# Kernel tuning notes

Hardware: AMD Instinct MI355X
Metric: run time of the kernel (lower is better)

Reference implementation:

```python
import jax, jax.numpy as jnp
import numpy as np

B, N, C, K1, K2, TD = 4, 4096, 128, 16, 8, 64
CIN = 2 * (3 + C)  # 262


def setup_inputs() -> dict:
    key = jax.random.key(0)
    ks = jax.random.split(key, 8)
    s = 0.05
    feature = jax.random.normal(ks[0], (B, C, N), jnp.float32)
    xyz = jax.random.normal(ks[1], (B, 3, N), jnp.float32)
    wq = jax.random.normal(ks[2], (TD, CIN), jnp.float32) * s
    wk = jax.random.normal(ks[3], (TD, CIN), jnp.float32) * s
    wv = jax.random.normal(ks[4], (TD, CIN), jnp.float32) * s
    w1 = jax.random.normal(ks[5], (C, TD), jnp.float32) * s
    bq = jnp.zeros((TD,), jnp.float32)
    bk = jnp.zeros((TD,), jnp.float32)
    bv = jnp.zeros((TD,), jnp.float32)
    b1 = jnp.zeros((C,), jnp.float32)
    return {"feature": feature, "xyz": xyz, "wq": wq, "bq": bq,
            "wk": wk, "bk": bk, "wv": wv, "bv": bv, "w1": w1, "b1": b1}


def _group(x, ind):
    # x: [B, Cx, N], ind: [B, N, K] -> [B, Cx, K, N]; g[b,c,k,n] = x[b,c,ind[b,n,k]]
    g = jnp.take_along_axis(x[:, :, None, :], ind[:, None, :, :], axis=3)  # [B,Cx,N,K]
    return g.transpose(0, 1, 3, 2)


def reference(feature, xyz, wq, bq, wk, bk, wv, bv, w1, b1):
    # --- KNN (self-included then dropped), idx[b,n,k] = k-th nearest of point n ---
    sq = jnp.sum(xyz * xyz, axis=1)                                   # [B,N]
    dist = sq[:, :, None] + sq[:, None, :] - 2.0 * jnp.einsum('bdn,bdm->bnm', xyz, xyz)
    _, idx = jax.lax.top_k(-dist, K1 + 1)                             # [B,N,17]
    idx = idx[:, :, 1:]                                               # drop self -> [B,N,16]
    idx1 = idx[:, :, :K2]                                             # [B,N,8]

    gxyz = _group(xyz, idx)        # [B,3,16,N]
    gxyz1 = _group(xyz, idx1)      # [B,3,8,N]
    gfea = _group(feature, idx)    # [B,C,16,N]
    gfea1 = _group(feature, idx1)  # [B,C,8,N]

    rel_xyz = gxyz - xyz[:, :, None, :]
    rel_xyz1 = gxyz1 - xyz[:, :, None, :]
    rel_fea = gfea - feature[:, :, None, :]
    rel_fea1 = gfea1 - feature[:, :, None, :]

    def relpos(rx, rf, K):
        return jnp.concatenate([
            rx,
            jnp.broadcast_to(xyz[:, :, None, :], (B, 3, K, N)),
            rf,
            jnp.broadcast_to(feature[:, :, None, :], (B, C, K, N)),
        ], axis=1)  # [B,262,K,N]

    rel_pos = relpos(rel_xyz, rel_fea, K1)     # [B,262,16,N]
    rel_pos1 = relpos(rel_xyz1, rel_fea1, K2)  # [B,262,8,N]

    # 1x1 Conv2d projections
    q = jnp.einsum('oc,bckn->bokn', wq, rel_pos1) + bq[None, :, None, None]  # [B,64,8,N]
    k = jnp.einsum('oc,bckn->bokn', wk, rel_pos) + bk[None, :, None, None]   # [B,64,16,N]
    v = jnp.einsum('oc,bckn->bokn', wv, rel_pos) + bv[None, :, None, None]   # [B,64,16,N]

    attn = jnp.einsum('bmnf,bmjf->bnjf', q, k)   # [B,8,16,N]
    attn = jax.nn.softmax(attn, axis=-2)         # softmax over j (16 neighbors)
    res = jnp.einsum('bnjf,bmjf->bmf', attn, v)  # [B,64,N]

    out = jnp.einsum('om,bmf->bof', w1, res) + b1[None, :, None]  # Conv1d 64->128
    return out + feature
```

## Files before the change

kernel.cpp:

```cpp
#include <hip/hip_runtime.h>

#define NN 4096
#define CCH 128

__global__ __launch_bounds__(256) void transpose_w(
    const float* __restrict__ wq, const float* __restrict__ wk, const float* __restrict__ wv,
    const float* __restrict__ w1,
    float* __restrict__ wTq, float* __restrict__ wTk, float* __restrict__ wTv,
    float* __restrict__ w1T, float* __restrict__ wPack) {
  int t = blockIdx.x * 256 + threadIdx.x;
  if (t < 64 * 262) {
    int o = t / 262, c = t - o * 262;
    wTq[c * 64 + o] = wq[t];
    wTk[c * 64 + o] = wk[t];
    wTv[c * 64 + o] = wv[t];
  }
  if (t < 128 * 64) {
    int r = t >> 6, c2 = t & 63;
    w1T[c2 * 128 + r] = w1[t];
  }
  if (t < 49152) {
    int r = t & 3, o = (t >> 2) & 63;
    int g = t >> 8;
    int ct = g / 6, mh = g - ct * 6;
    int m = mh >> 1, h = mh & 1;
    const float* wsrc = (m == 0) ? wq : ((m == 1) ? wk : wv);
    wPack[t] = wsrc[o * 262 + (h ? 134 : 6) + 4 * ct + r];
  }
}

__global__ __launch_bounds__(1024, 4) void knn_kernel(const float* __restrict__ xyz,
                                                      int* __restrict__ idxout) {
  __shared__ float4 pts[NN];
  __shared__ float sdist[16 * 16 * 64];
  __shared__ unsigned long long hits[32 * 64];
  __shared__ int cnt[64];
  const int b  = blockIdx.x >> 6;
  const int n0 = (blockIdx.x & 63) << 6;
  const float* xb = xyz + (size_t)b * 3 * NN;
  for (int i = threadIdx.x; i < NN; i += 1024) {
    float x = xb[i], y = xb[NN + i], z = xb[2 * NN + i];
    pts[i] = make_float4(x, y, z, x * x + y * y + z * z);
  }
  const int ql = threadIdx.x & 63;
  const int ch = threadIdx.x >> 6;
  if (threadIdx.x < 64) cnt[threadIdx.x] = 0;
  __syncthreads();
  const int q = n0 + ql;
  const float4 me = pts[q];
  float bd[16];
#pragma unroll
  for (int j = 0; j < 16; ++j) bd[j] = 3.0e38f;
  const int m0 = ch << 8, m1 = m0 + 256;
  for (int mb = m0; mb < m1; mb += 8) {
    float4 P[8];
#pragma unroll
    for (int u = 0; u < 8; ++u) P[u] = pts[mb + u];
#pragma unroll
    for (int u = 0; u < 8; ++u) {
      float d = me.w + P[u].w - 2.0f * (me.x * P[u].x + me.y * P[u].y + me.z * P[u].z);
      d = (mb + u == q) ? 3.0e38f : d;
#pragma unroll
      for (int j = 15; j >= 1; --j) bd[j] = __builtin_amdgcn_fmed3f(d, bd[j - 1], bd[j]);
      bd[0] = fminf(bd[0], d);
    }
  }
#pragma unroll
  for (int j = 0; j < 16; ++j) sdist[(ch * 16 + j) * 64 + ql] = bd[j];
  __syncthreads();
#pragma unroll
  for (int lvl = 0; lvl < 4; ++lvl) {
    const int nmerge = 8 >> lvl;
    float outv[16];
    const bool active = (ch < nmerge);
    if (active) {
      const float* A  = &sdist[((2 * ch) * 16) * 64 + ql];
      const float* Bp = &sdist[((2 * ch + 1) * 16) * 64 + ql];
      int pa = 0, pb = 0;
#pragma unroll
      for (int k = 0; k < 16; ++k) {
        float va = A[pa * 64], vb = Bp[pb * 64];
        bool takea = va <= vb;
        outv[k] = takea ? va : vb;
        pa += takea ? 1 : 0;
        pb += takea ? 0 : 1;
      }
    }
    __syncthreads();
    if (active) {
#pragma unroll
      for (int k = 0; k < 16; ++k) sdist[(ch * 16 + k) * 64 + ql] = outv[k];
    }
    __syncthreads();
  }
  const float tau = sdist[15 * 64 + ql];
  for (int mb = m0; mb < m1; mb += 8) {
    float4 P[8];
#pragma unroll
    for (int u = 0; u < 8; ++u) P[u] = pts[mb + u];
#pragma unroll
    for (int u = 0; u < 8; ++u) {
      float d = me.w + P[u].w - 2.0f * (me.x * P[u].x + me.y * P[u].y + me.z * P[u].z);
      if (d <= tau && (mb + u) != q) {
        int pos = atomicAdd(&cnt[ql], 1);
        if (pos < 32) {
          unsigned int f = __float_as_uint(d);
          f ^= (f >> 31) ? 0xFFFFFFFFu : 0x80000000u;
          hits[pos * 64 + ql] = ((unsigned long long)f << 32) | (unsigned int)(mb + u);
        }
      }
    }
  }
  __syncthreads();
  if (threadIdx.x < 64) {
    const int qq = threadIdx.x;
    int n = cnt[qq]; n = n > 32 ? 32 : n;
    unsigned long long kd[16];
#pragma unroll
    for (int j = 0; j < 16; ++j) kd[j] = ~0ULL;
    for (int t = 0; t < n; ++t) {
      unsigned long long key = hits[t * 64 + qq];
#pragma unroll
      for (int j = 15; j >= 1; --j) {
        bool up   = key < kd[j - 1];
        bool here = key < kd[j];
        kd[j] = up ? kd[j - 1] : (here ? key : kd[j]);
      }
      kd[0] = key < kd[0] ? key : kd[0];
    }
    int* op = idxout + ((size_t)((b << 12) + n0 + qq)) * 16;
#pragma unroll
    for (int k = 0; k < 16; ++k) op[k] = (int)(kd[k] & 0xFFFFFFFFu);
  }
}

__global__ __launch_bounds__(256, 4) void proj_kernel(
    const float* __restrict__ feature, const float* __restrict__ xyz,
    const float* __restrict__ wTq, const float* __restrict__ wTk, const float* __restrict__ wTv,
    const float* __restrict__ wPack,
    const float* __restrict__ bq, const float* __restrict__ bk, const float* __restrict__ bv,
    float* __restrict__ uq, float* __restrict__ cq,
    float* __restrict__ uk, float* __restrict__ ck,
    float* __restrict__ uv, float* __restrict__ cv) {
  __shared__ float fl[32][132];
  const int p0 = blockIdx.x << 5;
  const int b  = p0 >> 12;
  const int n0 = p0 & 4095;
  {
    const int i  = threadIdx.x & 31;
    const int c0 = threadIdx.x >> 5;
    const float* fb = feature + (size_t)b * CCH * NN + n0 + i;
    for (int cc = c0; cc < CCH; cc += 8) fl[i][cc] = fb[(size_t)cc * NN];
    if (threadIdx.x < 96) {
      const int d = threadIdx.x >> 5;
      fl[i][128 + d] = xyz[((size_t)b * 3 + d) * NN + n0 + i];
    }
  }
  __syncthreads();
  const int o  = threadIdx.x & 63;
  const int pg = threadIdx.x >> 6;
  const float4* wp = reinterpret_cast<const float4*>(wPack);
  float aU[3][8], aT[3][8];
#pragma unroll
  for (int mm = 0; mm < 3; ++mm)
#pragma unroll
    for (int s = 0; s < 8; ++s) { aU[mm][s] = 0.f; aT[mm][s] = 0.f; }
  for (int ct = 0; ct < 32; ++ct) {
    float4 w4[6];
#pragma unroll
    for (int mh = 0; mh < 6; ++mh) w4[mh] = wp[(ct * 6 + mh) * 64 + o];
#pragma unroll
    for (int s = 0; s < 8; ++s) {
      const float4 f4 = *reinterpret_cast<const float4*>(&fl[pg * 8 + s][4 * ct]);
#pragma unroll
      for (int mm = 0; mm < 3; ++mm) {
        aU[mm][s] += w4[2 * mm].x * f4.x + w4[2 * mm].y * f4.y + w4[2 * mm].z * f4.z + w4[2 * mm].w * f4.w;
        aT[mm][s] += w4[2 * mm + 1].x * f4.x + w4[2 * mm + 1].y * f4.y + w4[2 * mm + 1].z * f4.z + w4[2 * mm + 1].w * f4.w;
      }
    }
  }
  float wxu[3][3], wxt[3][3];
#pragma unroll
  for (int dd = 0; dd < 3; ++dd) {
    wxu[0][dd] = wTq[dd * 64 + o]; wxt[0][dd] = wTq[(3 + dd) * 64 + o];
    wxu[1][dd] = wTk[dd * 64 + o]; wxt[1][dd] = wTk[(3 + dd) * 64 + o];
    wxu[2][dd] = wTv[dd * 64 + o]; wxt[2][dd] = wTv[(3 + dd) * 64 + o];
  }
  const float bo0 = bq[o], bo1 = bk[o], bo2 = bv[o];
#pragma unroll
  for (int s = 0; s < 8; ++s) {
    const int p = pg * 8 + s;
    const float x = fl[p][128], y = fl[p][129], z = fl[p][130];
    const size_t gp = ((size_t)(p0 + p)) * 64 + o;
    float uu, tt;
    uu = aU[0][s] + wxu[0][0] * x + wxu[0][1] * y + wxu[0][2] * z;
    tt = aT[0][s] + wxt[0][0] * x + wxt[0][1] * y + wxt[0][2] * z;
    uq[gp] = uu; cq[gp] = tt + bo0 - uu;
    uu = aU[1][s] + wxu[1][0] * x + wxu[1][1] * y + wxu[1][2] * z;
    tt = aT[1][s] + wxt[1][0] * x + wxt[1][1] * y + wxt[1][2] * z;
    uk[gp] = uu; ck[gp] = tt + bo1 - uu;
    uu = aU[2][s] + wxu[2][0] * x + wxu[2][1] * y + wxu[2][2] * z;
    tt = aT[2][s] + wxt[2][0] * x + wxt[2][1] * y + wxt[2][2] * z;
    uv[gp] = uu; cv[gp] = tt + bo2 - uu;
  }
}

__global__ __launch_bounds__(256) void attn_core(
    const int* __restrict__ idx,
    const float* __restrict__ uq, const float* __restrict__ cq,
    const float* __restrict__ uk, const float* __restrict__ ck,
    const float* __restrict__ uv, const float* __restrict__ cv,
    float* __restrict__ res_ws) {
  __shared__ float kq[4][24][68];
  const int slot = threadIdx.x >> 6;
  const int o    = threadIdx.x & 63;
  const int p = (blockIdx.x << 2) + slot;
  const int b = p >> 12;
  const int myidx = idx[(size_t)p * 16 + (o & 15)];
  const size_t pb = (size_t)p * 64 + o;
  const float cqo = cq[pb], cko = ck[pb], cvo = cv[pb];
  const int rowbase = (b << 12) * 64;
  float v[16];
#pragma unroll
  for (int j = 0; j < 16; ++j) {
    int nb = __shfl(myidx, j);
    int row = rowbase + nb * 64 + o;
    kq[slot][j][o] = uk[row] + cko;
    v[j] = uv[row] + cvo;
    if (j < 8) kq[slot][16 + j][o] = uq[row] + cqo;
  }
  const int i  = o >> 3;
  const int jj = o & 7;
  const float* qrow = &kq[slot][16 + i][0];
  const float* k0r  = &kq[slot][jj][0];
  const float* k1r  = &kq[slot][8 + jj][0];
  float s0 = 0.f, s1 = 0.f;
#pragma unroll
  for (int t = 0; t < 16; ++t) {
    float4 q4 = *reinterpret_cast<const float4*>(qrow + 4 * t);
    float4 a4 = *reinterpret_cast<const float4*>(k0r + 4 * t);
    float4 c4 = *reinterpret_cast<const float4*>(k1r + 4 * t);
    s0 += q4.x * a4.x + q4.y * a4.y + q4.z * a4.z + q4.w * a4.w;
    s1 += q4.x * c4.x + q4.y * c4.y + q4.z * c4.z + q4.w * c4.w;
  }
  float mx = fmaxf(s0, s1);
  mx = fmaxf(mx, __shfl_xor(mx, 1));
  mx = fmaxf(mx, __shfl_xor(mx, 2));
  mx = fmaxf(mx, __shfl_xor(mx, 4));
  float e0 = __expf(s0 - mx), e1 = __expf(s1 - mx);
  float den = e0 + e1;
  den += __shfl_xor(den, 1);
  den += __shfl_xor(den, 2);
  den += __shfl_xor(den, 4);
  const float inv = 1.0f / den;
  float w0 = e0 * inv, w1s = e1 * inv;
  w0 += __shfl_xor(w0, 8);   w1s += __shfl_xor(w1s, 8);
  w0 += __shfl_xor(w0, 16);  w1s += __shfl_xor(w1s, 16);
  w0 += __shfl_xor(w0, 32);  w1s += __shfl_xor(w1s, 32);
  float res = 0.f;
#pragma unroll
  for (int j = 0; j < 8; ++j) {
    res += __shfl(w0, j)  * v[j];
    res += __shfl(w1s, j) * v[j + 8];
  }
  res_ws[pb] = res;
}

__global__ __launch_bounds__(256) void out_kernel(
    const float* __restrict__ feature, const float* __restrict__ res,
    const float* __restrict__ w1T, const float* __restrict__ b1,
    float* __restrict__ out) {
  __shared__ float rT[64][66];
  const int p0 = blockIdx.x << 6;
  const int b  = p0 >> 12;
  const int n0 = p0 & 4095;
  {
    const int o = threadIdx.x & 63;
    for (int pp = threadIdx.x >> 6; pp < 64; pp += 4)
      rT[o][pp] = res[(size_t)(p0 + pp) * 64 + o];
  }
  __syncthreads();
  const int n = threadIdx.x & 63;
  const int c0 = (threadIdx.x >> 6) * 32;
  float acc[32];
#pragma unroll
  for (int cc = 0; cc < 32; ++cc) acc[cc] = b1[c0 + cc];
  for (int o = 0; o < 64; ++o) {
    const float rr = rT[o][n];
    const float* wrow = &w1T[o * 128 + c0];
#pragma unroll
    for (int cc = 0; cc < 32; ++cc) acc[cc] += wrow[cc] * rr;
  }
#pragma unroll
  for (int cc = 0; cc < 32; ++cc) {
    const size_t gi = ((size_t)(b * 128 + c0 + cc) << 12) + n0 + n;
    out[gi] = acc[cc] + feature[gi];
  }
}

extern "C" void kernel_launch(void* const* d_in, const int* in_sizes, int n_in,
                              void* d_out, int out_size, void* d_ws, size_t ws_size,
                              hipStream_t stream) {
  const float* feature = (const float*)d_in[0];
  const float* xyz     = (const float*)d_in[1];
  const float* wq      = (const float*)d_in[2];
  const float* bq      = (const float*)d_in[3];
  const float* wk      = (const float*)d_in[4];
  const float* bk      = (const float*)d_in[5];
  const float* wv      = (const float*)d_in[6];
  const float* bv      = (const float*)d_in[7];
  const float* w1      = (const float*)d_in[8];
  const float* b1      = (const float*)d_in[9];
  float* out = (float*)d_out;

  char* ws = (char*)d_ws;
  int*   idx = (int*)ws;
  float* uq  = (float*)(ws + (1u << 20));
  float* cq  = uq + (1u << 20);
  float* uk  = cq + (1u << 20);
  float* ck  = uk + (1u << 20);
  float* uv  = ck + (1u << 20);
  float* cv  = uv + (1u << 20);
  float* res = cv + (1u << 20);
  float* wTq = res + (1u << 20);
  float* wTk = wTq + 262 * 64;
  float* wTv = wTk + 262 * 64;
  float* w1T = wTv + 262 * 64;
  float* wPk = w1T + 128 * 64;

  transpose_w<<<192, 256, 0, stream>>>(wq, wk, wv, w1, wTq, wTk, wTv, w1T, wPk);
  knn_kernel<<<256, 1024, 0, stream>>>(xyz, idx);
  proj_kernel<<<512, 256, 0, stream>>>(feature, xyz, wTq, wTk, wTv, wPk, bq, bk, bv,
                                       uq, cq, uk, ck, uv, cv);
  attn_core<<<4096, 256, 0, stream>>>(idx, uq, cq, uk, ck, uv, cv, res);
  out_kernel<<<256, 256, 0, stream>>>(feature, res, w1T, b1, out);
}
```

Before: 230.8 us.

## Track top-4 per KNN chunk, read points from global, prefetch proj weights

The KNN kernel now keeps only a 4-deep sorted list per 256-point chunk instead of 16, then merges the 16 chunk lists through a staged merge tree to derive the distance threshold tau. This cuts the per-candidate fmed3 insertion chain from 15 steps to 3. Point coordinates are packed once as float4 into a workspace buffer by the weight-transpose kernel. KNN reads them from global memory instead of staging 64 KB in LDS, which should raise occupancy. The projection kernel also software-prefetches the next weight tile into registers. The threshold taken from the merged top-4 lists is only an upper bound on the true 16th distance, so more candidates may pass the second scan and could overflow the 32-entry hit buffer.

```diff
diff --git a/kernel.cpp b/kernel.cpp
--- a/kernel.cpp
+++ b/kernel.cpp
@@ -5,9 +5,9 @@
 
 __global__ __launch_bounds__(256) void transpose_w(
     const float* __restrict__ wq, const float* __restrict__ wk, const float* __restrict__ wv,
-    const float* __restrict__ w1,
+    const float* __restrict__ w1, const float* __restrict__ xyz,
     float* __restrict__ wTq, float* __restrict__ wTk, float* __restrict__ wTv,
-    float* __restrict__ w1T, float* __restrict__ wPack) {
+    float* __restrict__ w1T, float* __restrict__ wPack, float4* __restrict__ pts4) {
   int t = blockIdx.x * 256 + threadIdx.x;
   if (t < 64 * 262) {
     int o = t / 262, c = t - o * 262;
@@ -27,77 +27,112 @@
     const float* wsrc = (m == 0) ? wq : ((m == 1) ? wk : wv);
     wPack[t] = wsrc[o * 262 + (h ? 134 : 6) + 4 * ct + r];
   }
-}
-
-__global__ __launch_bounds__(1024, 4) void knn_kernel(const float* __restrict__ xyz,
+  if (t < 4 * NN) {
+    int bb = t >> 12, i = t & 4095;
+    const float* xb = xyz + (size_t)bb * 3 * NN;
+    float x = xb[i], y = xb[NN + i], z = xb[2 * NN + i];
+    pts4[t] = make_float4(x, y, z, x * x + y * y + z * z);
+  }
+}
+
+__global__ __launch_bounds__(1024, 4) void knn_kernel(const float4* __restrict__ pts4,
                                                       int* __restrict__ idxout) {
-  __shared__ float4 pts[NN];
-  __shared__ float sdist[16 * 16 * 64];
+  __shared__ float bufA[64 * 64];
+  __shared__ float bufB[64 * 64];
   __shared__ unsigned long long hits[32 * 64];
   __shared__ int cnt[64];
   const int b  = blockIdx.x >> 6;
   const int n0 = (blockIdx.x & 63) << 6;
-  const float* xb = xyz + (size_t)b * 3 * NN;
-  for (int i = threadIdx.x; i < NN; i += 1024) {
-    float x = xb[i], y = xb[NN + i], z = xb[2 * NN + i];
-    pts[i] = make_float4(x, y, z, x * x + y * y + z * z);
-  }
   const int ql = threadIdx.x & 63;
-  const int ch = threadIdx.x >> 6;
+  const int ch = __builtin_amdgcn_readfirstlane(threadIdx.x >> 6);
   if (threadIdx.x < 64) cnt[threadIdx.x] = 0;
-  __syncthreads();
   const int q = n0 + ql;
-  const float4 me = pts[q];
-  float bd[16];
-#pragma unroll
-  for (int j = 0; j < 16; ++j) bd[j] = 3.0e38f;
-  const int m0 = ch << 8, m1 = m0 + 256;
-  for (int mb = m0; mb < m1; mb += 8) {
+  const float4* pb4 = pts4 + ((size_t)b << 12);
+  const float4 me = pb4[q];
+  float bd0 = 3.0e38f, bd1 = 3.0e38f, bd2 = 3.0e38f, bd3 = 3.0e38f;
+  const int m0 = ch << 8;
+  for (int mb = m0; mb < m0 + 256; mb += 8) {
     float4 P[8];
 #pragma unroll
-    for (int u = 0; u < 8; ++u) P[u] = pts[mb + u];
+    for (int u = 0; u < 8; ++u) P[u] = pb4[mb + u];
 #pragma unroll
     for (int u = 0; u < 8; ++u) {
       float d = me.w + P[u].w - 2.0f * (me.x * P[u].x + me.y * P[u].y + me.z * P[u].z);
       d = (mb + u == q) ? 3.0e38f : d;
-#pragma unroll
-      for (int j = 15; j >= 1; --j) bd[j] = __builtin_amdgcn_fmed3f(d, bd[j - 1], bd[j]);
-      bd[0] = fminf(bd[0], d);
-    }
-  }
-#pragma unroll
-  for (int j = 0; j < 16; ++j) sdist[(ch * 16 + j) * 64 + ql] = bd[j];
-  __syncthreads();
-#pragma unroll
-  for (int lvl = 0; lvl < 4; ++lvl) {
-    const int nmerge = 8 >> lvl;
-    float outv[16];
-    const bool active = (ch < nmerge);
-    if (active) {
-      const float* A  = &sdist[((2 * ch) * 16) * 64 + ql];
-      const float* Bp = &sdist[((2 * ch + 1) * 16) * 64 + ql];
-      int pa = 0, pb = 0;
-#pragma unroll
-      for (int k = 0; k < 16; ++k) {
-        float va = A[pa * 64], vb = Bp[pb * 64];
-        bool takea = va <= vb;
-        outv[k] = takea ? va : vb;
-        pa += takea ? 1 : 0;
-        pb += takea ? 0 : 1;
-      }
-    }
-    __syncthreads();
-    if (active) {
-#pragma unroll
-      for (int k = 0; k < 16; ++k) sdist[(ch * 16 + k) * 64 + ql] = outv[k];
-    }
-    __syncthreads();
-  }
-  const float tau = sdist[15 * 64 + ql];
-  for (int mb = m0; mb < m1; mb += 8) {
+      bd3 = __builtin_amdgcn_fmed3f(d, bd2, bd3);
+      bd2 = __builtin_amdgcn_fmed3f(d, bd1, bd2);
+      bd1 = __builtin_amdgcn_fmed3f(d, bd0, bd1);
+      bd0 = fminf(bd0, d);
+    }
+  }
+  {
+    const int r0 = (ch * 4) * 64 + ql;
+    bufA[r0] = bd0; bufA[r0 + 64] = bd1; bufA[r0 + 128] = bd2; bufA[r0 + 192] = bd3;
+  }
+  __syncthreads();
+  if (ch < 8) {
+    const int a0 = (2 * ch) * 4, b0 = (2 * ch + 1) * 4;
+    float o8[8]; int pa = 0, pb = 0;
+#pragma unroll
+    for (int k = 0; k < 8; ++k) {
+      float va = (pa < 4) ? bufA[(a0 + pa) * 64 + ql] : 3.0e38f;
+      float vb = (pb < 4) ? bufA[(b0 + pb) * 64 + ql] : 3.0e38f;
+      bool ta = va <= vb;
+      o8[k] = ta ? va : vb;
+      pa += ta ? 1 : 0; pb += ta ? 0 : 1;
+    }
+#pragma unroll
+    for (int k = 0; k < 8; ++k) bufB[(ch * 8 + k) * 64 + ql] = o8[k];
+  }
+  __syncthreads();
+  if (ch < 4) {
+    const int a0 = (2 * ch) * 8, b0 = (2 * ch + 1) * 8;
+    float o16[16]; int pa = 0, pb = 0;
+#pragma unroll
+    for (int k = 0; k < 16; ++k) {
+      float va = (pa < 8) ? bufB[(a0 + pa) * 64 + ql] : 3.0e38f;
+      float vb = (pb < 8) ? bufB[(b0 + pb) * 64 + ql] : 3.0e38f;
+      bool ta = va <= vb;
+      o16[k] = ta ? va : vb;
+      pa += ta ? 1 : 0; pb += ta ? 0 : 1;
+    }
+#pragma unroll
+    for (int k = 0; k < 16; ++k) bufA[(ch * 16 + k) * 64 + ql] = o16[k];
+  }
+  __syncthreads();
+  if (ch < 2) {
+    const int a0 = (2 * ch) * 16, b0 = (2 * ch + 1) * 16;
+    float o16[16]; int pa = 0, pb = 0;
+#pragma unroll
+    for (int k = 0; k < 16; ++k) {
+      float va = bufA[(a0 + pa) * 64 + ql];
+      float vb = bufA[(b0 + pb) * 64 + ql];
+      bool ta = va <= vb;
+      o16[k] = ta ? va : vb;
+      pa += ta ? 1 : 0; pb += ta ? 0 : 1;
+    }
+#pragma unroll
+    for (int k = 0; k < 16; ++k) bufB[(ch * 16 + k) * 64 + ql] = o16[k];
+  }
+  __syncthreads();
+  if (ch == 0) {
+    float v = 0.f; int pa = 0, pb = 0;
+#pragma unroll
+    for (int k = 0; k < 16; ++k) {
+      float va = bufB[pa * 64 + ql];
+      float vb = bufB[(16 + pb) * 64 + ql];
+      bool ta = va <= vb;
+      v = ta ? va : vb;
+      pa += ta ? 1 : 0; pb += ta ? 0 : 1;
+    }
+    bufA[15 * 64 + ql] = v;
+  }
+  __syncthreads();
+  const float tau = bufA[15 * 64 + ql];
+  for (int mb = m0; mb < m0 + 256; mb += 8) {
     float4 P[8];
 #pragma unroll
-    for (int u = 0; u < 8; ++u) P[u] = pts[mb + u];
+    for (int u = 0; u < 8; ++u) P[u] = pb4[mb + u];
 #pragma unroll
     for (int u = 0; u < 8; ++u) {
       float d = me.w + P[u].w - 2.0f * (me.x * P[u].x + me.y * P[u].y + me.z * P[u].z);
@@ -165,10 +200,14 @@
   for (int mm = 0; mm < 3; ++mm)
 #pragma unroll
     for (int s = 0; s < 8; ++s) { aU[mm][s] = 0.f; aT[mm][s] = 0.f; }
+  float4 w4[6];
+#pragma unroll
+  for (int mh = 0; mh < 6; ++mh) w4[mh] = wp[mh * 64 + o];
   for (int ct = 0; ct < 32; ++ct) {
-    float4 w4[6];
-#pragma unroll
-    for (int mh = 0; mh < 6; ++mh) w4[mh] = wp[(ct * 6 + mh) * 64 + o];
+    float4 w4n[6];
+    const int ctn = (ct + 1) & 31;
+#pragma unroll
+    for (int mh = 0; mh < 6; ++mh) w4n[mh] = wp[(ctn * 6 + mh) * 64 + o];
 #pragma unroll
     for (int s = 0; s < 8; ++s) {
       const float4 f4 = *reinterpret_cast<const float4*>(&fl[pg * 8 + s][4 * ct]);
@@ -178,6 +217,8 @@
         aT[mm][s] += w4[2 * mm + 1].x * f4.x + w4[2 * mm + 1].y * f4.y + w4[2 * mm + 1].z * f4.z + w4[2 * mm + 1].w * f4.w;
       }
     }
+#pragma unroll
+    for (int mh = 0; mh < 6; ++mh) w4[mh] = w4n[mh];
   }
   float wxu[3][3], wxt[3][3];
 #pragma unroll
@@ -314,8 +355,9 @@
   float* out = (float*)d_out;
 
   char* ws = (char*)d_ws;
-  int*   idx = (int*)ws;
-  float* uq  = (float*)(ws + (1u << 20));
+  int*    idx  = (int*)ws;
+  float4* pts4 = (float4*)(ws + (1u << 20));
+  float* uq  = (float*)(ws + (2u << 20));
   float* cq  = uq + (1u << 20);
   float* uk  = cq + (1u << 20);
   float* ck  = uk + (1u << 20);
@@ -328,8 +370,8 @@
   float* w1T = wTv + 262 * 64;
   float* wPk = w1T + 128 * 64;
 
-  transpose_w<<<192, 256, 0, stream>>>(wq, wk, wv, w1, wTq, wTk, wTv, w1T, wPk);
-  knn_kernel<<<256, 1024, 0, stream>>>(xyz, idx);
+  transpose_w<<<192, 256, 0, stream>>>(wq, wk, wv, w1, xyz, wTq, wTk, wTv, w1T, wPk, pts4);
+  knn_kernel<<<256, 1024, 0, stream>>>(pts4, idx);
   proj_kernel<<<512, 256, 0, stream>>>(feature, xyz, wTq, wTk, wTv, wPk, bq, bk, bv,
                                        uq, cq, uk, ck, uv, cv);
   attn_core<<<4096, 256, 0, stream>>>(idx, uq, cq, uk, ck, uv, cv, res);
```

After: 264.9 us. 1.15x slower.
